# Kernel optimization log

Measured on AMD Instinct MI355X. Metric: run time of the kernel, lower is better.

Reference implementation:

```python
import jax, jax.numpy as jnp
import numpy as np

D_MODEL = 1024
H = 16
D_K = D_MODEL // H
WINDOW = 256
NEG = -1e9


def setup_inputs() -> dict:
    key = jax.random.key(0)
    ks = jax.random.split(key, 7)
    B, S = 2, 4096
    sc = 0.02
    return {
        "q": jax.random.normal(ks[0], (B, S, D_MODEL), jnp.float32),
        "k": jax.random.normal(ks[1], (B, S, D_MODEL), jnp.float32),
        "v": jax.random.normal(ks[2], (B, S, D_MODEL), jnp.float32),
        "wq": jax.random.normal(ks[3], (D_MODEL, D_MODEL), jnp.float32) * sc,
        "wk": jax.random.normal(ks[4], (D_MODEL, D_MODEL), jnp.float32) * sc,
        "wv": jax.random.normal(ks[5], (D_MODEL, D_MODEL), jnp.float32) * sc,
        "wo": jax.random.normal(ks[6], (D_MODEL, D_MODEL), jnp.float32) * sc,
    }


def _local_mask(seq_len: int, window_size: int):
    left = (window_size - 1) // 2
    right = window_size - 1 - left
    idx = jnp.arange(seq_len)
    dist = jnp.abs(idx[None, :] - idx[:, None])
    return (dist <= left) | (dist <= right)  # [S, S] bool


def reference(q, k, v, wq, wk, wv, wo):
    B, S, _ = q.shape
    # torch Linear: x @ W.T
    def proj(x, w):
        return (x @ w.T).reshape(B, S, H, D_K).transpose(0, 2, 1, 3)  # [B,H,S,Dk]
    Q, K, V = proj(q, wq), proj(k, wk), proj(v, wv)
    scores = jnp.einsum("bhqd,bhkd->bhqk", Q, K) / jnp.sqrt(jnp.float32(D_K))
    mask = _local_mask(S, WINDOW)
    scores = jnp.where(mask[None, None], scores, NEG)
    attn = jax.nn.softmax(scores, axis=-1)
    x = jnp.einsum("bhqk,bhkd->bhqd", attn, V)
    x = x.transpose(0, 2, 1, 3).reshape(B, S, D_MODEL)
    return x @ wo.T
```

## Files before the change

### kernel.cpp

```cpp
#include <hip/hip_runtime.h>
#include <hip/hip_bf16.h>

#define S_LEN 4096
#define B_SZ 2
#define DM 1024
#define NH 16
#define DH 64

typedef __attribute__((ext_vector_type(8))) short short8;
typedef __attribute__((ext_vector_type(4))) float f32x4;

__device__ __forceinline__ ushort f2b(float f) {
  union { __hip_bfloat16 b; ushort u; } cv;
  cv.b = __float2bfloat16(f);
  return cv.u;
}

__device__ __forceinline__ void glds16(const ushort* g, ushort* l) {
  __builtin_amdgcn_global_load_lds(
      (const __attribute__((address_space(1))) void*)g,
      (__attribute__((address_space(3))) void*)l, 16, 0, 0);
}

__global__ void cvt_all(const float* __restrict__ q, const float* __restrict__ k,
                        const float* __restrict__ v, const float* __restrict__ wq,
                        const float* __restrict__ wk, const float* __restrict__ wv,
                        const float* __restrict__ wo, ushort* __restrict__ dst) {
  const int NX4 = 2097152;
  const int NW4 = 262144;
  const int total = 3 * NX4 + 4 * NW4;
  for (int i = blockIdx.x * blockDim.x + threadIdx.x; i < total;
       i += gridDim.x * blockDim.x) {
    const float* s;
    int j;
    if (i < NX4) { s = q; j = i; }
    else if (i < 2 * NX4) { s = k; j = i - NX4; }
    else if (i < 3 * NX4) { s = v; j = i - 2 * NX4; }
    else {
      int t = i - 3 * NX4;
      int wsel = t >> 18;
      j = t & (NW4 - 1);
      s = wsel == 0 ? wq : wsel == 1 ? wk : wsel == 2 ? wv : wo;
    }
    float4 val = reinterpret_cast<const float4*>(s)[j];
    ushort4 o;
    o.x = f2b(val.x); o.y = f2b(val.y); o.z = f2b(val.z); o.w = f2b(val.w);
    reinterpret_cast<ushort4*>(dst)[i] = o;
  }
}

__device__ __forceinline__ short8 ldsrd(const ushort* base, int row, int cb) {
  const int pcb = cb ^ ((row & 7) << 4);
  return *reinterpret_cast<const short8*>(
      reinterpret_cast<const char*>(base) + row * 128 + pcb);
}

template <int MODE>
__launch_bounds__(512, 2)
__global__ void gemm8(const ushort* __restrict__ A0, const ushort* __restrict__ A1,
                      const ushort* __restrict__ A2, const ushort* __restrict__ W0,
                      const ushort* __restrict__ W1, const ushort* __restrict__ W2,
                      void* __restrict__ O0, void* __restrict__ O1,
                      void* __restrict__ O2) {
  __shared__ ushort As[2][16384];
  __shared__ ushort Bs[2][16384];
  const int tid = threadIdx.x;
  const int lane = tid & 63, w = tid >> 6;
  const int g = lane >> 4, lr = lane & 15;
  const int m0 = blockIdx.x * 256;
  const int ysel = (MODE == 0) ? (blockIdx.y >> 2) : 0;
  const ushort* A = (MODE == 0) ? (ysel == 0 ? A0 : ysel == 1 ? A1 : A2) : A0;
  const ushort* W = (MODE == 0) ? (ysel == 0 ? W0 : ysel == 1 ? W1 : W2) : W0;
  const int n0 = ((MODE == 0) ? (blockIdx.y & 3) : blockIdx.y) * 256;

  const int row_r = tid >> 3;
  const int cb = ((tid & 7) * 16) ^ ((row_r & 7) << 4);
  const ushort* Asrc = A + (size_t)(m0 + row_r) * DM + (cb >> 1);
  const ushort* Wsrc = W + (size_t)(n0 + row_r) * DM + (cb >> 1);

#define STG_A(buf, kt, h)                                                     \
  { const int kq = (kt) * 64;                                                 \
    glds16(Asrc + (size_t)((h) * 128) * DM + kq, &As[buf][(h) * 8192 + w * 512]); \
    glds16(Asrc + (size_t)((h) * 128 + 64) * DM + kq,                         \
           &As[buf][(h) * 8192 + 4096 + w * 512]); }
#define STG_B(buf, kt, h)                                                     \
  { const int kq = (kt) * 64;                                                 \
    glds16(Wsrc + (size_t)((h) * 128) * DM + kq, &Bs[buf][(h) * 8192 + w * 512]); \
    glds16(Wsrc + (size_t)((h) * 128 + 64) * DM + kq,                         \
           &Bs[buf][(h) * 8192 + 4096 + w * 512]); }

  f32x4 acc[16][2] = {};
  short8 af[4][2], bf[2][2];

  STG_B(0, 0, 0); STG_B(0, 0, 1); STG_A(0, 0, 0); STG_A(0, 0, 1);
  asm volatile("s_waitcnt vmcnt(2)" ::: "memory");
  __builtin_amdgcn_s_barrier();
  __builtin_amdgcn_sched_barrier(0);

  for (int kt = 0; kt < 16; ++kt) {
    const int buf = kt & 1;
    const int tn = kt < 15 ? kt + 1 : 15;
    const ushort* Acur = &As[buf][0];
    const ushort* Bcur = &Bs[buf][0];
#pragma unroll
    for (int p = 0; p < 4; ++p) {
      if (p == 0) {
#pragma unroll
        for (int n = 0; n < 2; n++)
#pragma unroll
          for (int kk = 0; kk < 2; kk++)
            bf[n][kk] = ldsrd(Bcur, w * 32 + n * 16 + lr, kk * 64 + g * 16);
      }
#pragma unroll
      for (int i = 0; i < 4; i++)
#pragma unroll
        for (int kk = 0; kk < 2; kk++)
          af[i][kk] = ldsrd(Acur, (4 * p + i) * 16 + lr, kk * 64 + g * 16);
      if (p == 0)      { STG_B(buf ^ 1, tn, 0); }
      else if (p == 1) { STG_B(buf ^ 1, tn, 1); }
      else if (p == 2) { STG_A(buf ^ 1, tn, 0); }
      else             { STG_A(buf ^ 1, tn, 1); }
      if (p == 1) asm volatile("s_waitcnt vmcnt(4)" ::: "memory");
      if (p == 3) asm volatile("s_waitcnt vmcnt(2)" ::: "memory");
      __builtin_amdgcn_sched_barrier(0);
      __builtin_amdgcn_s_barrier();
      asm volatile("s_waitcnt lgkmcnt(0)" ::: "memory");
      __builtin_amdgcn_sched_barrier(0);
      __builtin_amdgcn_s_setprio(1);
#pragma unroll
      for (int i = 0; i < 4; i++)
#pragma unroll
        for (int n = 0; n < 2; n++)
#pragma unroll
          for (int kk = 0; kk < 2; kk++)
            acc[4 * p + i][n] = __builtin_amdgcn_mfma_f32_16x16x32_bf16(
                af[i][kk], bf[n][kk], acc[4 * p + i][n], 0, 0, 0);
      __builtin_amdgcn_s_setprio(0);
      __builtin_amdgcn_sched_barrier(0);
      __builtin_amdgcn_s_barrier();
    }
  }
#undef STG_A
#undef STG_B

  const int colB = n0 + w * 32;
#pragma unroll
  for (int m = 0; m < 16; ++m) {
    const int row0 = m0 + m * 16 + g * 4;
#pragma unroll
    for (int n = 0; n < 2; ++n) {
      const int col = colB + n * 16 + lr;
      if (MODE == 2) {
#pragma unroll
        for (int r = 0; r < 4; r++)
          reinterpret_cast<float*>(O0)[(size_t)(row0 + r) * DM + col] = acc[m][n][r];
      } else if (ysel == 0 || ysel == 1) {
        ushort* O = reinterpret_cast<ushort*>(ysel == 0 ? O0 : O1);
#pragma unroll
        for (int r = 0; r < 4; r++)
          O[(size_t)(row0 + r) * DM + col] = f2b(acc[m][n][r]);
      } else {
        const int b = row0 >> 12, s0 = row0 & 4095;
        const int h = col >> 6, dk = col & 63;
        ushort4 o;
        o.x = f2b(acc[m][n][0]); o.y = f2b(acc[m][n][1]);
        o.z = f2b(acc[m][n][2]); o.w = f2b(acc[m][n][3]);
        *reinterpret_cast<ushort4*>(
            reinterpret_cast<ushort*>(O2) +
            (((size_t)(b * NH + h) * DH + dk) << 12) + s0) = o;
      }
    }
  }
}

__global__ void attn_local(const ushort* __restrict__ Qp, const ushort* __restrict__ Kp,
                           const ushort* __restrict__ Vt, ushort* __restrict__ Ao) {
  __shared__ ushort Ks[64 * 64];
  __shared__ ushort Vs[64 * 64];
  __shared__ ushort Ps[4][16 * 72];
  const int tid = threadIdx.x;
  const int lane = tid & 63;
  const int w = tid >> 6;
  const int g = lane >> 4, lr = lane & 15;
  const int bh = blockIdx.y, b = bh >> 4, h = bh & 15;
  const int q0 = blockIdx.x * 64;

  const int qrow = q0 + w * 16 + lr;
  const ushort* qptr = Qp + ((size_t)b * S_LEN + qrow) * DM + h * DH;
  short8 qf[2];
  qf[0] = *reinterpret_cast<const short8*>(qptr + g * 8);
  qf[1] = *reinterpret_cast<const short8*>(qptr + 32 + g * 8);

  float m_r[4], l_r[4];
  f32x4 acc_o[4] = {};
#pragma unroll
  for (int r = 0; r < 4; r++) { m_r[r] = -1e30f; l_r[r] = 0.f; }

  const int sr = tid >> 3;
  const int scb = (tid & 7) * 16;

  const int t_lo = q0 >= 128 ? q0 - 128 : 0;
  const int t_hi = (q0 + 192) <= S_LEN ? (q0 + 192) : S_LEN;

  for (int k0 = t_lo; k0 < t_hi; k0 += 64) {
    __syncthreads();
#pragma unroll
    for (int i = 0; i < 2; i++) {
      const int row = i * 32 + sr;
      const int cb = scb ^ ((row & 7) << 4);
      glds16(Kp + ((size_t)b * S_LEN + k0 + row) * DM + h * DH + cb / 2,
             Ks + i * 2048 + w * 512);
      glds16(Vt + (((size_t)bh * DH + row) << 12) + k0 + cb / 2,
             Vs + i * 2048 + w * 512);
    }
    __syncthreads();

    f32x4 sc[4] = {};
#pragma unroll
    for (int kk = 0; kk < 2; kk++) {
#pragma unroll
      for (int nt = 0; nt < 4; nt++) {
        const int kr = nt * 16 + lr;
        const int cb = (kk * 64 + g * 16) ^ ((kr & 7) << 4);
        short8 kf = *reinterpret_cast<const short8*>(
            reinterpret_cast<const char*>(Ks) + kr * 128 + cb);
        sc[nt] = __builtin_amdgcn_mfma_f32_16x16x32_bf16(qf[kk], kf, sc[nt], 0, 0, 0);
      }
    }
    float mx[4] = {-1e30f, -1e30f, -1e30f, -1e30f};
#pragma unroll
    for (int nt = 0; nt < 4; nt++) {
      const int key = k0 + nt * 16 + lr;
#pragma unroll
      for (int r = 0; r < 4; r++) {
        const int qr = q0 + w * 16 + g * 4 + r;
        int d = qr - key; d = d < 0 ? -d : d;
        float s = (d <= 128) ? sc[nt][r] * 0.125f : -1e9f;
        sc[nt][r] = s;
        mx[r] = fmaxf(mx[r], s);
      }
    }
#pragma unroll
    for (int r = 0; r < 4; r++) {
      mx[r] = fmaxf(mx[r], __shfl_xor(mx[r], 1));
      mx[r] = fmaxf(mx[r], __shfl_xor(mx[r], 2));
      mx[r] = fmaxf(mx[r], __shfl_xor(mx[r], 4));
      mx[r] = fmaxf(mx[r], __shfl_xor(mx[r], 8));
    }
    float fac[4], rs[4];
#pragma unroll
    for (int r = 0; r < 4; r++) {
      const float mn = fmaxf(m_r[r], mx[r]);
      fac[r] = __expf(m_r[r] - mn);
      m_r[r] = mn;
      rs[r] = 0.f;
    }
#pragma unroll
    for (int nt = 0; nt < 4; nt++)
#pragma unroll
      for (int r = 0; r < 4; r++) {
        const float p = __expf(sc[nt][r] - m_r[r]);
        sc[nt][r] = p;
        rs[r] += p;
      }
#pragma unroll
    for (int r = 0; r < 4; r++) {
      rs[r] += __shfl_xor(rs[r], 1);
      rs[r] += __shfl_xor(rs[r], 2);
      rs[r] += __shfl_xor(rs[r], 4);
      rs[r] += __shfl_xor(rs[r], 8);
      l_r[r] = l_r[r] * fac[r] + rs[r];
    }
#pragma unroll
    for (int nt = 0; nt < 4; nt++)
#pragma unroll
      for (int r = 0; r < 4; r++)
        acc_o[nt][r] *= fac[r];

    ushort* myP = Ps[w];
#pragma unroll
    for (int nt = 0; nt < 4; nt++)
#pragma unroll
      for (int r = 0; r < 4; r++)
        myP[(g * 4 + r) * 72 + nt * 16 + lr] = f2b(sc[nt][r]);
    asm volatile("s_waitcnt lgkmcnt(0)" ::: "memory");
    __builtin_amdgcn_sched_barrier(0);

#pragma unroll
    for (int kk = 0; kk < 2; kk++) {
      short8 pf = *reinterpret_cast<const short8*>(myP + lr * 72 + kk * 32 + g * 8);
#pragma unroll
      for (int nt = 0; nt < 4; nt++) {
        const int vr = nt * 16 + lr;
        const int cb = (kk * 64 + g * 16) ^ ((vr & 7) << 4);
        short8 vf = *reinterpret_cast<const short8*>(
            reinterpret_cast<const char*>(Vs) + vr * 128 + cb);
        acc_o[nt] = __builtin_amdgcn_mfma_f32_16x16x32_bf16(pf, vf, acc_o[nt], 0, 0, 0);
      }
    }
  }

  const int qr0 = q0 + w * 16 + g * 4;
  ushort* orow = Ao + (size_t)b * S_LEN * DM + h * DH;
#pragma unroll
  for (int nt = 0; nt < 4; nt++)
#pragma unroll
    for (int r = 0; r < 4; r++)
      orow[(size_t)(qr0 + r) * DM + nt * 16 + lr] = f2b(acc_o[nt][r] / l_r[r]);
}

extern "C" void kernel_launch(void* const* d_in, const int* in_sizes, int n_in,
                              void* d_out, int out_size, void* d_ws, size_t ws_size,
                              hipStream_t stream) {
  const float* q  = (const float*)d_in[0];
  const float* k  = (const float*)d_in[1];
  const float* v  = (const float*)d_in[2];
  const float* wq = (const float*)d_in[3];
  const float* wk = (const float*)d_in[4];
  const float* wv = (const float*)d_in[5];
  const float* wo = (const float*)d_in[6];

  const size_t NX = (size_t)B_SZ * S_LEN * DM;
  const size_t NW = (size_t)DM * DM;
  if (ws_size < (7 * NX + 4 * NW) * sizeof(ushort)) return;

  ushort* ws  = (ushort*)d_ws;
  ushort* qb  = ws;
  ushort* kb  = qb + NX;
  ushort* vb  = kb + NX;
  ushort* wqb = vb + NX;
  ushort* wkb = wqb + NW;
  ushort* wvb = wkb + NW;
  ushort* wob = wvb + NW;
  ushort* Qp  = wob + NW;
  ushort* Kp  = Qp + NX;
  ushort* Vt  = Kp + NX;
  ushort* Ao  = Vt + NX;

  cvt_all<<<dim3(2048), dim3(256), 0, stream>>>(q, k, v, wq, wk, wv, wo, ws);

  gemm8<0><<<dim3(32, 12), dim3(512), 0, stream>>>(qb, kb, vb, wqb, wkb, wvb,
                                                   Qp, Kp, Vt);

  attn_local<<<dim3(64, 32), dim3(256), 0, stream>>>(Qp, Kp, Vt, Ao);

  gemm8<2><<<dim3(32, 4), dim3(512), 0, stream>>>(Ao, Ao, Ao, wob, wob, wob,
                                                  d_out, d_out, d_out);
}
```

Measured before the change: 173.6 us.

## Restructure GEMM to 256x128 tiles with triple-buffered prefetch and 4x2 warp grid

Replaces the 256x256 double-buffered GEMM with a 256x128 tile, a 3-stage LDS ring that prefetches two k-steps ahead, and a 4x2 warp layout in which each warp computes a 64x64 sub-tile. Each k-step is split into two halves that interleave global-to-LDS staging with MFMA work and use fewer barriers. The grid doubles, which improves occupancy and load balance across CUs, at the cost of more re-reads of A and some added complexity in the vmcnt accounting.

```diff
diff --git a/kernel.cpp b/kernel.cpp
--- a/kernel.cpp
+++ b/kernel.cpp
@@ -57,98 +57,110 @@
 
 template <int MODE>
 __launch_bounds__(512, 2)
-__global__ void gemm8(const ushort* __restrict__ A0, const ushort* __restrict__ A1,
+__global__ void gemmP(const ushort* __restrict__ A0, const ushort* __restrict__ A1,
                       const ushort* __restrict__ A2, const ushort* __restrict__ W0,
                       const ushort* __restrict__ W1, const ushort* __restrict__ W2,
                       void* __restrict__ O0, void* __restrict__ O1,
                       void* __restrict__ O2) {
-  __shared__ ushort As[2][16384];
-  __shared__ ushort Bs[2][16384];
+  __shared__ ushort As[3][16384];
+  __shared__ ushort Bs[3][8192];
   const int tid = threadIdx.x;
   const int lane = tid & 63, w = tid >> 6;
+  const int wm = w >> 1, wn = w & 1;
   const int g = lane >> 4, lr = lane & 15;
   const int m0 = blockIdx.x * 256;
-  const int ysel = (MODE == 0) ? (blockIdx.y >> 2) : 0;
+  const int ysel = (MODE == 0) ? (blockIdx.y >> 3) : 0;
   const ushort* A = (MODE == 0) ? (ysel == 0 ? A0 : ysel == 1 ? A1 : A2) : A0;
   const ushort* W = (MODE == 0) ? (ysel == 0 ? W0 : ysel == 1 ? W1 : W2) : W0;
-  const int n0 = ((MODE == 0) ? (blockIdx.y & 3) : blockIdx.y) * 256;
+  const int n0 = ((MODE == 0) ? (blockIdx.y & 7) : blockIdx.y) * 128;
 
   const int row_r = tid >> 3;
   const int cb = ((tid & 7) * 16) ^ ((row_r & 7) << 4);
   const ushort* Asrc = A + (size_t)(m0 + row_r) * DM + (cb >> 1);
   const ushort* Wsrc = W + (size_t)(n0 + row_r) * DM + (cb >> 1);
 
-#define STG_A(buf, kt, h)                                                     \
-  { const int kq = (kt) * 64;                                                 \
-    glds16(Asrc + (size_t)((h) * 128) * DM + kq, &As[buf][(h) * 8192 + w * 512]); \
-    glds16(Asrc + (size_t)((h) * 128 + 64) * DM + kq,                         \
-           &As[buf][(h) * 8192 + 4096 + w * 512]); }
-#define STG_B(buf, kt, h)                                                     \
-  { const int kq = (kt) * 64;                                                 \
-    glds16(Wsrc + (size_t)((h) * 128) * DM + kq, &Bs[buf][(h) * 8192 + w * 512]); \
-    glds16(Wsrc + (size_t)((h) * 128 + 64) * DM + kq,                         \
-           &Bs[buf][(h) * 8192 + 4096 + w * 512]); }
-
-  f32x4 acc[16][2] = {};
+#define STG_A012(bs, kt)                                                     \
+  { const int kq = (kt) * 64;                                                \
+    glds16(Asrc + kq,                        &As[bs][w * 512]);              \
+    glds16(Asrc + (size_t)64 * DM + kq,      &As[bs][4096 + w * 512]);       \
+    glds16(Asrc + (size_t)128 * DM + kq,     &As[bs][8192 + w * 512]); }
+#define STG_A3B01(bs, kt)                                                    \
+  { const int kq = (kt) * 64;                                                \
+    glds16(Asrc + (size_t)192 * DM + kq,     &As[bs][12288 + w * 512]);      \
+    glds16(Wsrc + kq,                        &Bs[bs][w * 512]);              \
+    glds16(Wsrc + (size_t)64 * DM + kq,      &Bs[bs][4096 + w * 512]); }
+
+  f32x4 acc[4][4] = {};
   short8 af[4][2], bf[2][2];
 
-  STG_B(0, 0, 0); STG_B(0, 0, 1); STG_A(0, 0, 0); STG_A(0, 0, 1);
-  asm volatile("s_waitcnt vmcnt(2)" ::: "memory");
-  __builtin_amdgcn_s_barrier();
-  __builtin_amdgcn_sched_barrier(0);
-
+  STG_A012(0, 0); STG_A3B01(0, 0);
+  STG_A012(1, 1); STG_A3B01(1, 1);
+
+  int bc = 0;
   for (int kt = 0; kt < 16; ++kt) {
-    const int buf = kt & 1;
-    const int tn = kt < 15 ? kt + 1 : 15;
-    const ushort* Acur = &As[buf][0];
-    const ushort* Bcur = &Bs[buf][0];
-#pragma unroll
-    for (int p = 0; p < 4; ++p) {
-      if (p == 0) {
-#pragma unroll
-        for (int n = 0; n < 2; n++)
-#pragma unroll
-          for (int kk = 0; kk < 2; kk++)
-            bf[n][kk] = ldsrd(Bcur, w * 32 + n * 16 + lr, kk * 64 + g * 16);
-      }
-#pragma unroll
-      for (int i = 0; i < 4; i++)
+    const int bs = bc >= 1 ? bc - 1 : bc + 2;
+    const int tn = kt + 2 < 16 ? kt + 2 : 15;
+    asm volatile("s_waitcnt vmcnt(6)" ::: "memory");
+    __builtin_amdgcn_s_barrier();
+    __builtin_amdgcn_sched_barrier(0);
+    const ushort* Ab = &As[bc][0];
+    const ushort* Bb = &Bs[bc][0];
+#pragma unroll
+    for (int m = 0; m < 4; m++)
+#pragma unroll
+      for (int kk = 0; kk < 2; kk++)
+        af[m][kk] = ldsrd(Ab, wm * 64 + m * 16 + lr, kk * 64 + g * 16);
+#pragma unroll
+    for (int n = 0; n < 2; n++)
+#pragma unroll
+      for (int kk = 0; kk < 2; kk++)
+        bf[n][kk] = ldsrd(Bb, wn * 64 + n * 16 + lr, kk * 64 + g * 16);
+    STG_A012(bs, tn);
+    __builtin_amdgcn_sched_barrier(0);
+    asm volatile("s_waitcnt lgkmcnt(0)" ::: "memory");
+    __builtin_amdgcn_sched_barrier(0);
+    __builtin_amdgcn_s_setprio(1);
+#pragma unroll
+    for (int m = 0; m < 4; m++)
+#pragma unroll
+      for (int n = 0; n < 2; n++)
 #pragma unroll
         for (int kk = 0; kk < 2; kk++)
-          af[i][kk] = ldsrd(Acur, (4 * p + i) * 16 + lr, kk * 64 + g * 16);
-      if (p == 0)      { STG_B(buf ^ 1, tn, 0); }
-      else if (p == 1) { STG_B(buf ^ 1, tn, 1); }
-      else if (p == 2) { STG_A(buf ^ 1, tn, 0); }
-      else             { STG_A(buf ^ 1, tn, 1); }
-      if (p == 1) asm volatile("s_waitcnt vmcnt(4)" ::: "memory");
-      if (p == 3) asm volatile("s_waitcnt vmcnt(2)" ::: "memory");
-      __builtin_amdgcn_sched_barrier(0);
-      __builtin_amdgcn_s_barrier();
-      asm volatile("s_waitcnt lgkmcnt(0)" ::: "memory");
-      __builtin_amdgcn_sched_barrier(0);
-      __builtin_amdgcn_s_setprio(1);
-#pragma unroll
-      for (int i = 0; i < 4; i++)
-#pragma unroll
-        for (int n = 0; n < 2; n++)
-#pragma unroll
-          for (int kk = 0; kk < 2; kk++)
-            acc[4 * p + i][n] = __builtin_amdgcn_mfma_f32_16x16x32_bf16(
-                af[i][kk], bf[n][kk], acc[4 * p + i][n], 0, 0, 0);
-      __builtin_amdgcn_s_setprio(0);
-      __builtin_amdgcn_sched_barrier(0);
-      __builtin_amdgcn_s_barrier();
-    }
+          acc[m][n] = __builtin_amdgcn_mfma_f32_16x16x32_bf16(af[m][kk], bf[n][kk],
+                                                              acc[m][n], 0, 0, 0);
+    __builtin_amdgcn_s_setprio(0);
+    __builtin_amdgcn_sched_barrier(0);
+#pragma unroll
+    for (int n = 0; n < 2; n++)
+#pragma unroll
+      for (int kk = 0; kk < 2; kk++)
+        bf[n][kk] = ldsrd(Bb, wn * 64 + 32 + n * 16 + lr, kk * 64 + g * 16);
+    STG_A3B01(bs, tn);
+    __builtin_amdgcn_sched_barrier(0);
+    asm volatile("s_waitcnt lgkmcnt(0)" ::: "memory");
+    __builtin_amdgcn_sched_barrier(0);
+    __builtin_amdgcn_s_setprio(1);
+#pragma unroll
+    for (int m = 0; m < 4; m++)
+#pragma unroll
+      for (int n = 0; n < 2; n++)
+#pragma unroll
+        for (int kk = 0; kk < 2; kk++)
+          acc[m][2 + n] = __builtin_amdgcn_mfma_f32_16x16x32_bf16(af[m][kk], bf[n][kk],
+                                                                  acc[m][2 + n], 0, 0, 0);
+    __builtin_amdgcn_s_setprio(0);
+    __builtin_amdgcn_sched_barrier(0);
+    bc = bc + 1 == 3 ? 0 : bc + 1;
   }
-#undef STG_A
-#undef STG_B
-
-  const int colB = n0 + w * 32;
-#pragma unroll
-  for (int m = 0; m < 16; ++m) {
-    const int row0 = m0 + m * 16 + g * 4;
-#pragma unroll
-    for (int n = 0; n < 2; ++n) {
+#undef STG_A012
+#undef STG_A3B01
+
+  const int colB = n0 + wn * 64;
+#pragma unroll
+  for (int m = 0; m < 4; ++m) {
+    const int row0 = m0 + wm * 64 + m * 16 + g * 4;
+#pragma unroll
+    for (int n = 0; n < 4; ++n) {
       const int col = colB + n * 16 + lr;
       if (MODE == 2) {
 #pragma unroll
@@ -339,11 +351,11 @@
 
   cvt_all<<<dim3(2048), dim3(256), 0, stream>>>(q, k, v, wq, wk, wv, wo, ws);
 
-  gemm8<0><<<dim3(32, 12), dim3(512), 0, stream>>>(qb, kb, vb, wqb, wkb, wvb,
+  gemmP<0><<<dim3(32, 24), dim3(512), 0, stream>>>(qb, kb, vb, wqb, wkb, wvb,
                                                    Qp, Kp, Vt);
 
   attn_local<<<dim3(64, 32), dim3(256), 0, stream>>>(Qp, Kp, Vt, Ao);
 
-  gemm8<2><<<dim3(32, 4), dim3(512), 0, stream>>>(Ao, Ao, Ao, wob, wob, wob,
+  gemmP<2><<<dim3(32, 8), dim3(512), 0, stream>>>(Ao, Ao, Ao, wob, wob, wob,
                                                   d_out, d_out, d_out);
 }
```

After: 154.8 us. 10.8% less time.
